# Performance work log

Measured on AMD Instinct MI355X. Metric: run time of the kernel, lower is better.

The kernel has to match this reference:

```python
import jax, jax.numpy as jnp
import numpy as np

N_NODES = 10000
IN_SIZE, H_SIZE, OUT_SIZE = 512, 512, 64
N_EDGES = 163840


def gcn_conv(x, edge_index, W, b, n_nodes):
    """PyG-style GCNConv: add self-loops, sym-normalize, x @ W, scatter-add, + bias."""
    src, dst = edge_index[0], edge_index[1]
    loop = jnp.arange(n_nodes, dtype=src.dtype)
    src = jnp.concatenate([src, loop])
    dst = jnp.concatenate([dst, loop])
    # degree over destinations (self-loops included)
    deg = jax.ops.segment_sum(jnp.ones_like(dst, dtype=x.dtype), dst, num_segments=n_nodes)
    dinv = jnp.where(deg > 0, jax.lax.rsqrt(deg), 0.0)
    norm = dinv[src] * dinv[dst]                      # [E+N]
    h = x @ W                                          # [N, out]
    msg = h[src] * norm[:, None]                       # gather + scale
    out = jax.ops.segment_sum(msg, dst, num_segments=n_nodes)  # scatter-add
    return out + b


def setup_inputs() -> dict:
    key = jax.random.key(0)
    k = jax.random.split(key, 6)
    x = jax.random.normal(k[0], (N_NODES, IN_SIZE), dtype=jnp.float32)
    edge_index = jax.random.randint(k[1], (2, N_EDGES), 0, N_NODES, dtype=jnp.int64 if jax.config.read('jax_enable_x64') else jnp.int32)
    # Glorot-ish init for weights, zero bias (PyG default)
    W1 = jax.random.normal(k[2], (IN_SIZE, H_SIZE), dtype=jnp.float32) * (1.0 / np.sqrt(IN_SIZE))
    b1 = jnp.zeros((H_SIZE,), dtype=jnp.float32)
    W2 = jax.random.normal(k[3], (H_SIZE, OUT_SIZE), dtype=jnp.float32) * (1.0 / np.sqrt(H_SIZE))
    b2 = jnp.zeros((OUT_SIZE,), dtype=jnp.float32)
    return {"x": x, "edge_index": edge_index, "W1": W1, "b1": b1, "W2": W2, "b2": b2}


def reference(x, edge_index, W1, b1, W2, b2):
    n = x.shape[0]
    h = gcn_conv(x, edge_index, W1, b1, n)
    h = jax.nn.relu(h)
    h = gcn_conv(h, edge_index, W2, b2, n)
    return (h, jax.nn.log_softmax(h, axis=1))
```

## Files before the change

### kernel.cpp

```cpp
#include <hip/hip_runtime.h>
#include <math.h>

#define NN 10000
#define INF 512
#define HF  512
#define OF  64
#define NE  163840
#define MAXDEG 64

typedef __attribute__((ext_vector_type(8))) short bf16x8_t;
typedef __attribute__((ext_vector_type(4))) float f32x4_t;

__device__ inline ushort f2bf(float f) {
    unsigned u = __float_as_uint(f);
    u = (u + 0x7FFF + ((u >> 16) & 1)) >> 16;
    return (ushort)u;
}
__device__ inline float bf2f(ushort u) {
    return __uint_as_float(((unsigned)u) << 16);
}

#define GLL(gp, lp) __builtin_amdgcn_global_load_lds(                         \
    (const __attribute__((address_space(1))) unsigned int*)(gp),              \
    (__attribute__((address_space(3))) unsigned int*)(lp), 16, 0, 0)

#define CCB_X  2500
#define CCB_W1 2756
#define CCB_W2 2788
#define CCB_Z  2828
__global__ __launch_bounds__(256) void k_cvt(const float* __restrict__ X,
                                             ushort* __restrict__ Xb,
                                             const float* __restrict__ W1,
                                             ushort* __restrict__ W1T,
                                             const float* __restrict__ W2,
                                             ushort* __restrict__ W2T,
                                             int* __restrict__ gdeg) {
    __shared__ float tl[32][33];
    int b = blockIdx.x, t = threadIdx.x;
    if (b < CCB_X) {
        int i = (b * 256 + t) * 2;
        const float4* Xv = (const float4*)X;
        float4 v0 = Xv[i], v1 = Xv[i + 1];
        ushort4 o0, o1;
        o0.x = f2bf(v0.x); o0.y = f2bf(v0.y); o0.z = f2bf(v0.z); o0.w = f2bf(v0.w);
        o1.x = f2bf(v1.x); o1.y = f2bf(v1.y); o1.z = f2bf(v1.z); o1.w = f2bf(v1.w);
        ((ushort4*)Xb)[i] = o0;
        ((ushort4*)Xb)[i + 1] = o1;
    } else if (b < CCB_W2) {
        const float* W; ushort* WT; int N, tile;
        if (b < CCB_W1) { W = W1; WT = W1T; N = 512; tile = b - CCB_X; }
        else            { W = W2; WT = W2T; N = 64;  tile = b - CCB_W1; }
        int k0 = (tile & 15) * 32;
        int n0 = (tile >> 4) * 32;
        int tx = t & 31, ty = t >> 5;
#pragma unroll
        for (int i = 0; i < 4; i++)
            tl[ty + i * 8][tx] = W[(size_t)(k0 + ty + i * 8) * N + n0 + tx];
        __syncthreads();
#pragma unroll
        for (int i = 0; i < 4; i++)
            WT[(size_t)(n0 + ty + i * 8) * 512 + k0 + tx] = f2bf(tl[tx][ty + i * 8]);
    } else {
        int i = (b - CCB_W2) * 256 + t;
        if (i < NN) gdeg[i] = 0;
    }
}

#define GEMM_B 316
__global__ __launch_bounds__(256) void k_gemm_ell(const ushort* __restrict__ Xb,
                                                  const ushort* __restrict__ WT,
                                                  ushort* __restrict__ Y,
                                                  const int* __restrict__ src,
                                                  const int* __restrict__ dst,
                                                  int* __restrict__ gdeg,
                                                  int* __restrict__ ell, int E) {
    __shared__ ushort As[128 * 128];
    __shared__ ushort Bs[128 * 128];
    int b = blockIdx.x;
    int tid = threadIdx.x;
    if (b >= GEMM_B) {
        int e = (b - GEMM_B) * 256 + tid;
        if (e < E) {
            int s = src[e], d = dst[e];
            int r = atomicAdd(&gdeg[d], 1);
            if (r < MAXDEG) ell[d * MAXDEG + r] = s;
        }
        return;
    }
    int lane = tid & 63;
    int wave = tid >> 6;
    int m = lane & 15;
    int q = lane >> 4;
    int wr = wave >> 1;
    int wc = wave & 1;
    int row0 = (b % 79) * 128;
    int col0 = (b / 79) * 128;

    int lrow = lane >> 4;
    int p = lane & 15;
    int koff[4];
#pragma unroll
    for (int jm = 0; jm < 4; jm++) koff[jm] = (p ^ ((jm * 4 + lrow) & 15)) * 8;

    f32x4_t acc[4][4];
#pragma unroll
    for (int r = 0; r < 4; r++)
#pragma unroll
        for (int c = 0; c < 4; c++) acc[r][c] = (f32x4_t){0.f, 0.f, 0.f, 0.f};

    for (int kb = 0; kb < 512; kb += 128) {
#pragma unroll
        for (int j = 0; j < 8; j++) {
            int rloc = wave * 32 + j * 4;
            GLL(Xb + (size_t)(row0 + rloc + lrow) * 512 + kb + koff[j & 3],
                As + rloc * 128);
            GLL(WT + (size_t)(col0 + rloc + lrow) * 512 + kb + koff[j & 3],
                Bs + rloc * 128);
        }
        __syncthreads();
#pragma unroll
        for (int kc = 0; kc < 4; kc++) {
            bf16x8_t a[4], bb[4];
            int slot = ((kc * 4 + q) ^ m) * 8;
#pragma unroll
            for (int r = 0; r < 4; r++)
                a[r] = *(const bf16x8_t*)(As + (wr * 64 + r * 16 + m) * 128 + slot);
#pragma unroll
            for (int c = 0; c < 4; c++)
                bb[c] = *(const bf16x8_t*)(Bs + (wc * 64 + c * 16 + m) * 128 + slot);
#pragma unroll
            for (int r = 0; r < 4; r++)
#pragma unroll
                for (int c = 0; c < 4; c++)
                    acc[r][c] = __builtin_amdgcn_mfma_f32_16x16x32_bf16(a[r], bb[c], acc[r][c], 0, 0, 0);
        }
        __syncthreads();
    }
#pragma unroll
    for (int r = 0; r < 4; r++) {
#pragma unroll
        for (int c = 0; c < 4; c++) {
#pragma unroll
            for (int reg = 0; reg < 4; reg++) {
                int row = row0 + wr * 64 + r * 16 + q * 4 + reg;
                int col = col0 + wc * 64 + c * 16 + m;
                if (row < NN) Y[(size_t)row * 512 + col] = f2bf(acc[r][c][reg]);
            }
        }
    }
}

__global__ __launch_bounds__(256) void k_gemm64_mfma(const ushort* __restrict__ Ab,
                                                     const ushort* __restrict__ W2T,
                                                     ushort* __restrict__ Y) {
    __shared__ ushort As[64 * 128];
    __shared__ ushort Bs[64 * 128];
    int tid = threadIdx.x;
    int lane = tid & 63;
    int wave = tid >> 6;
    int m = lane & 15;
    int q = lane >> 4;
    int row0 = blockIdx.x * 64;

    int lrow = lane >> 4;
    int p = lane & 15;
    int koff[4];
#pragma unroll
    for (int jm = 0; jm < 4; jm++) koff[jm] = (p ^ ((jm * 4 + lrow) & 15)) * 8;

    f32x4_t acc[4];
#pragma unroll
    for (int c = 0; c < 4; c++) acc[c] = (f32x4_t){0.f, 0.f, 0.f, 0.f};

    for (int kb = 0; kb < 512; kb += 128) {
#pragma unroll
        for (int j = 0; j < 4; j++) {
            int rloc = wave * 16 + j * 4;
            GLL(Ab + (size_t)(row0 + rloc + lrow) * 512 + kb + koff[j],
                As + rloc * 128);
            GLL(W2T + (size_t)(rloc + lrow) * 512 + kb + koff[j],
                Bs + rloc * 128);
        }
        __syncthreads();
#pragma unroll
        for (int kc = 0; kc < 4; kc++) {
            int slot = ((kc * 4 + q) ^ m) * 8;
            bf16x8_t a = *(const bf16x8_t*)(As + (wave * 16 + m) * 128 + slot);
#pragma unroll
            for (int c = 0; c < 4; c++) {
                bf16x8_t bfr = *(const bf16x8_t*)(Bs + (c * 16 + m) * 128 + slot);
                acc[c] = __builtin_amdgcn_mfma_f32_16x16x32_bf16(a, bfr, acc[c], 0, 0, 0);
            }
        }
        __syncthreads();
    }
#pragma unroll
    for (int c = 0; c < 4; c++) {
#pragma unroll
        for (int reg = 0; reg < 4; reg++) {
            int row = row0 + wave * 16 + q * 4 + reg;
            int col = c * 16 + m;
            if (row < NN) Y[(size_t)row * 64 + col] = f2bf(acc[c][reg]);
        }
    }
}

__global__ __launch_bounds__(128) void k_agg1(const ushort* __restrict__ h1b,
                                              const int* __restrict__ gdeg,
                                              const int* __restrict__ ell,
                                              const float* __restrict__ b,
                                              ushort* __restrict__ a1b,
                                              float* __restrict__ wts) {
    __shared__ int   sidx[2][64];
    __shared__ float swt[2][64];
    int w = threadIdx.x >> 6;
    int t = threadIdx.x & 63;
    int v = blockIdx.x * 2 + w;
    int deg = gdeg[v]; if (deg > MAXDEG) deg = MAXDEG;
    float dv = rsqrtf((float)(deg + 1));
    int s = 0; float wt = 0.f;
    if (t < deg) {
        s = ell[v * MAXDEG + t];
        wt = rsqrtf((float)(gdeg[s] + 1)) * dv;
    }
    sidx[w][t] = s; swt[w][t] = wt;
    wts[v * MAXDEG + t] = wt;

    int fb = t * 8;
    float acc[8];
    {
        bf16x8_t su = *(const bf16x8_t*)(h1b + (size_t)v * 512 + fb);
        float dv2 = dv * dv;
#pragma unroll
        for (int f = 0; f < 8; f++) acc[f] = bf2f((ushort)su[f]) * dv2;
    }
    int nr = (deg + 3) & ~3;
    for (int i = 0; i < nr; i += 4) {
        bf16x8_t nb[4]; float wK[4];
#pragma unroll
        for (int k = 0; k < 4; k++) {
            int sK = sidx[w][i + k];
            wK[k] = swt[w][i + k];
            nb[k] = *(const bf16x8_t*)(h1b + (size_t)sK * 512 + fb);
        }
#pragma unroll
        for (int k = 0; k < 4; k++)
#pragma unroll
            for (int f = 0; f < 8; f++)
                acc[f] += bf2f((ushort)nb[k][f]) * wK[k];
    }
    bf16x8_t o;
#pragma unroll
    for (int f = 0; f < 8; f++) {
        float x = acc[f] + b[fb + f];
        o[f] = (short)f2bf(x > 0.f ? x : 0.f);
    }
    *(bf16x8_t*)(a1b + (size_t)v * 512 + fb) = o;
}

__global__ __launch_bounds__(256) void k_agg2_lsm(const ushort* __restrict__ h2b,
                                                  const int* __restrict__ gdeg,
                                                  const int* __restrict__ ell,
                                                  const float* __restrict__ wts,
                                                  const float* __restrict__ b,
                                                  float* __restrict__ out) {
    __shared__ int   sidx[4][64];
    __shared__ float swt[4][64];
    int t = threadIdx.x & 63;
    int w = threadIdx.x >> 6;
    int v = blockIdx.x * 4 + w;
    int deg = gdeg[v]; if (deg > MAXDEG) deg = MAXDEG;
    float dv = rsqrtf((float)(deg + 1));
    int   e_ = ell[v * MAXDEG + t];
    float w_ = wts[v * MAXDEG + t];
    sidx[w][t] = (t < deg) ? e_ : 0;
    swt[w][t]  = (t < deg) ? w_ : 0.f;

    float acc[8];
#pragma unroll
    for (int k = 0; k < 8; k++) acc[k] = 0.f;
    acc[0] = bf2f(h2b[(size_t)v * 64 + t]) * (dv * dv);

    int nr = (deg + 7) & ~7;
    for (int i = 0; i < nr; i += 8) {
        int   sK[8]; float wK[8];
#pragma unroll
        for (int k = 0; k < 8; k++) { sK[k] = sidx[w][i + k]; wK[k] = swt[w][i + k]; }
#pragma unroll
        for (int k = 0; k < 8; k++)
            acc[k] += bf2f(h2b[(size_t)sK[k] * 64 + t]) * wK[k];
    }
    float h = ((acc[0] + acc[1]) + (acc[2] + acc[3])) +
              ((acc[4] + acc[5]) + (acc[6] + acc[7]));
    h += b[t];
    out[(size_t)v * 64 + t] = h;
    float m = h;
#pragma unroll
    for (int off = 32; off >= 1; off >>= 1) m = fmaxf(m, __shfl_xor(m, off, 64));
    float e = expf(h - m);
    float ssum = e;
#pragma unroll
    for (int off = 32; off >= 1; off >>= 1) ssum += __shfl_xor(ssum, off, 64);
    out[(size_t)NN * OF + (size_t)v * 64 + t] = h - m - logf(ssum);
}


extern "C" void kernel_launch(void* const* d_in, const int* in_sizes, int n_in,
                              void* d_out, int out_size, void* d_ws, size_t ws_size,
                              hipStream_t stream) {
    const float* x  = (const float*)d_in[0];
    const int*   ei = (const int*)d_in[1];
    const float* W1 = (const float*)d_in[2];
    const float* b1 = (const float*)d_in[3];
    const float* W2 = (const float*)d_in[4];
    const float* b2 = (const float*)d_in[5];
    float* out = (float*)d_out;

    int E = in_sizes[1] / 2;
    const int* src = ei;
    const int* dst = ei + E;

    char* w = (char*)d_ws;
    auto carve = [&](size_t bytes) {
        char* p = w;
        w += (bytes + 255) & ~size_t(255);
        return p;
    };
    ushort* Xb     = (ushort*)carve((size_t)NN * 512 * 2);
    ushort* h1b    = (ushort*)carve((size_t)NN * 512 * 2);
    ushort* a1b    = (ushort*)carve((size_t)NN * 512 * 2);
    ushort* h2b    = (ushort*)carve((size_t)NN * 64 * 2);
    ushort* W1Tb   = (ushort*)carve((size_t)512 * 512 * 2);
    ushort* W2Tb   = (ushort*)carve((size_t)64 * 512 * 2);
    int*   gdeg    = (int*)carve((size_t)NN * 4);
    int*   ell     = (int*)carve((size_t)NN * MAXDEG * 4);
    float* wts     = (float*)carve((size_t)NN * MAXDEG * 4);
    (void)ws_size;

    int fillB = (E + 255) / 256;
    k_cvt<<<CCB_Z, 256, 0, stream>>>(x, Xb, W1, W1Tb, W2, W2Tb, gdeg);
    k_gemm_ell<<<GEMM_B + fillB, 256, 0, stream>>>(Xb, W1Tb, h1b, src, dst,
                                                   gdeg, ell, E);
    k_agg1<<<NN / 2, 128, 0, stream>>>(h1b, gdeg, ell, b1, a1b, wts);
    k_gemm64_mfma<<<(NN + 63) / 64, 256, 0, stream>>>(a1b, W2Tb, h2b);
    k_agg2_lsm<<<NN / 4, 256, 0, stream>>>(h2b, gdeg, ell, wts, b2, out);
}
```

Before: 129.6 us.

## Fuse layer-1 aggregation with layer-2 GEMM through LDS-staged rows

Merges the layer-1 aggregation kernel and the 512x64 second GEMM into one kernel. Each 512-thread block aggregates 8 nodes, writes the bf16 ReLU rows into swizzled LDS, and four waves then run MFMA against W2T read straight from global memory. This removes the a1b intermediate (a 10 MB write and read) and one kernel launch. In exchange, W2T is re-read per block without LDS staging, half of each 16-row MFMA tile is wasted on padding rows, and the larger blocks run at lower occupancy.

```diff
diff --git a/kernel.cpp b/kernel.cpp
--- a/kernel.cpp
+++ b/kernel.cpp
@@ -150,72 +150,20 @@
     }
 }
 
-__global__ __launch_bounds__(256) void k_gemm64_mfma(const ushort* __restrict__ Ab,
-                                                     const ushort* __restrict__ W2T,
-                                                     ushort* __restrict__ Y) {
-    __shared__ ushort As[64 * 128];
-    __shared__ ushort Bs[64 * 128];
-    int tid = threadIdx.x;
-    int lane = tid & 63;
-    int wave = tid >> 6;
-    int m = lane & 15;
-    int q = lane >> 4;
-    int row0 = blockIdx.x * 64;
-
-    int lrow = lane >> 4;
-    int p = lane & 15;
-    int koff[4];
-#pragma unroll
-    for (int jm = 0; jm < 4; jm++) koff[jm] = (p ^ ((jm * 4 + lrow) & 15)) * 8;
-
-    f32x4_t acc[4];
-#pragma unroll
-    for (int c = 0; c < 4; c++) acc[c] = (f32x4_t){0.f, 0.f, 0.f, 0.f};
-
-    for (int kb = 0; kb < 512; kb += 128) {
-#pragma unroll
-        for (int j = 0; j < 4; j++) {
-            int rloc = wave * 16 + j * 4;
-            GLL(Ab + (size_t)(row0 + rloc + lrow) * 512 + kb + koff[j],
-                As + rloc * 128);
-            GLL(W2T + (size_t)(rloc + lrow) * 512 + kb + koff[j],
-                Bs + rloc * 128);
-        }
-        __syncthreads();
-#pragma unroll
-        for (int kc = 0; kc < 4; kc++) {
-            int slot = ((kc * 4 + q) ^ m) * 8;
-            bf16x8_t a = *(const bf16x8_t*)(As + (wave * 16 + m) * 128 + slot);
-#pragma unroll
-            for (int c = 0; c < 4; c++) {
-                bf16x8_t bfr = *(const bf16x8_t*)(Bs + (c * 16 + m) * 128 + slot);
-                acc[c] = __builtin_amdgcn_mfma_f32_16x16x32_bf16(a, bfr, acc[c], 0, 0, 0);
-            }
-        }
-        __syncthreads();
-    }
-#pragma unroll
-    for (int c = 0; c < 4; c++) {
-#pragma unroll
-        for (int reg = 0; reg < 4; reg++) {
-            int row = row0 + wave * 16 + q * 4 + reg;
-            int col = c * 16 + m;
-            if (row < NN) Y[(size_t)row * 64 + col] = f2bf(acc[c][reg]);
-        }
-    }
-}
-
-__global__ __launch_bounds__(128) void k_agg1(const ushort* __restrict__ h1b,
-                                              const int* __restrict__ gdeg,
-                                              const int* __restrict__ ell,
-                                              const float* __restrict__ b,
-                                              ushort* __restrict__ a1b,
-                                              float* __restrict__ wts) {
-    __shared__ int   sidx[2][64];
-    __shared__ float swt[2][64];
+__global__ __launch_bounds__(512) void k_agg1_gemm2(const ushort* __restrict__ h1b,
+                                                    const int* __restrict__ gdeg,
+                                                    const int* __restrict__ ell,
+                                                    const float* __restrict__ b1,
+                                                    const ushort* __restrict__ W2T,
+                                                    ushort* __restrict__ h2b,
+                                                    float* __restrict__ wts) {
+    __shared__ ushort rlds[16 * 512];
+    __shared__ int   sidx[8][64];
+    __shared__ float swt[8][64];
     int w = threadIdx.x >> 6;
     int t = threadIdx.x & 63;
-    int v = blockIdx.x * 2 + w;
+    int v = blockIdx.x * 8 + w;
+
     int deg = gdeg[v]; if (deg > MAXDEG) deg = MAXDEG;
     float dv = rsqrtf((float)(deg + 1));
     int s = 0; float wt = 0.f;
@@ -252,10 +200,32 @@
     bf16x8_t o;
 #pragma unroll
     for (int f = 0; f < 8; f++) {
-        float x = acc[f] + b[fb + f];
+        float x = acc[f] + b1[fb + f];
         o[f] = (short)f2bf(x > 0.f ? x : 0.f);
     }
-    *(bf16x8_t*)(a1b + (size_t)v * 512 + fb) = o;
+    int slot = (t & 48) | ((t & 15) ^ w);
+    *(bf16x8_t*)(rlds + w * 512 + slot * 8) = o;
+    __syncthreads();
+
+    if (w >= 4) return;
+    int m = t & 15;
+    int q = t >> 4;
+    f32x4_t qa = (f32x4_t){0.f, 0.f, 0.f, 0.f};
+    const ushort* wrow = W2T + (size_t)(w * 16 + m) * 512;
+#pragma unroll
+    for (int ks = 0; ks < 16; ks++) {
+        int kg = ks * 4 + q;
+        int sl = (kg & 48) | ((kg & 15) ^ m);
+        bf16x8_t af  = *(const bf16x8_t*)(rlds + m * 512 + sl * 8);
+        bf16x8_t bfr = *(const bf16x8_t*)(wrow + ks * 32 + q * 8);
+        qa = __builtin_amdgcn_mfma_f32_16x16x32_bf16(af, bfr, qa, 0, 0, 0);
+    }
+#pragma unroll
+    for (int reg = 0; reg < 4; reg++) {
+        int rl = q * 4 + reg;
+        if (rl < 8)
+            h2b[(size_t)(blockIdx.x * 8 + rl) * 64 + w * 16 + m] = f2bf(qa[reg]);
+    }
 }
 
 __global__ __launch_bounds__(256) void k_agg2_lsm(const ushort* __restrict__ h2b,
@@ -328,7 +298,6 @@
     };
     ushort* Xb     = (ushort*)carve((size_t)NN * 512 * 2);
     ushort* h1b    = (ushort*)carve((size_t)NN * 512 * 2);
-    ushort* a1b    = (ushort*)carve((size_t)NN * 512 * 2);
     ushort* h2b    = (ushort*)carve((size_t)NN * 64 * 2);
     ushort* W1Tb   = (ushort*)carve((size_t)512 * 512 * 2);
     ushort* W2Tb   = (ushort*)carve((size_t)64 * 512 * 2);
@@ -341,7 +310,6 @@
     k_cvt<<<CCB_Z, 256, 0, stream>>>(x, Xb, W1, W1Tb, W2, W2Tb, gdeg);
     k_gemm_ell<<<GEMM_B + fillB, 256, 0, stream>>>(Xb, W1Tb, h1b, src, dst,
                                                    gdeg, ell, E);
-    k_agg1<<<NN / 2, 128, 0, stream>>>(h1b, gdeg, ell, b1, a1b, wts);
-    k_gemm64_mfma<<<(NN + 63) / 64, 256, 0, stream>>>(a1b, W2Tb, h2b);
+    k_agg1_gemm2<<<NN / 8, 512, 0, stream>>>(h1b, gdeg, ell, b1, W2Tb, h2b, wts);
     k_agg2_lsm<<<NN / 4, 256, 0, stream>>>(h2b, gdeg, ell, wts, b2, out);
 }
```

Result: no change. 131.1 us (+1.1%).
